# Kernel optimization log

Hardware: AMD Instinct MI355X
Metric: run time of the kernel (lower is better)

## Reference

```python
import jax, jax.numpy as jnp
import numpy as np

H = W = 64
ALPHA = 1.0
BETA = 100.0
LIMB_PAIRS = np.array([[0,1],[1,2],[2,3],[0,4],[4,5],[5,6],[0,7],[7,8],[8,9],[9,10],
                       [8,11],[11,12],[12,13],[8,14],[14,15],[15,16]])
P0 = LIMB_PAIRS[:, 0]
P1 = LIMB_PAIRS[:, 1]
_last = {}
for _l, _j in enumerate(P0):
    _last[int(_j)] = _l
J0 = np.array(list(_last.keys()))   # unique proximal joints
L0 = np.array(list(_last.values())) # last limb writing to each joint


def make_kernel(h, w, alpha):
    # replicates: coords = stack(meshgrid(arange(2h-1), arange(2w-1))).transpose(1,2) (h==w)
    ii, jj = jnp.meshgrid(jnp.arange(2 * h - 1), jnp.arange(2 * w - 1), indexing='ij')
    ker = jnp.stack([h - jj, w - ii], axis=0).astype(jnp.float32)  # (2, 2h-1, 2w-1)
    dist = jnp.linalg.norm(ker, axis=0, keepdims=True)
    dist = dist.at[0, h, w].set(1.0)
    return ker / dist ** (1.0 + alpha)


def corr_full(x, k):
    # x: (N, Cin, h, w); k: (Cout, Cin, 2h-1, 2w-1); 'same' correlation with pad h-1/w-1
    h, w = x.shape[-2:]
    return jax.lax.conv_general_dilated(x, k, (1, 1), ((h - 1, h - 1), (w - 1, w - 1)))


def heatmap_std(x, di=False):
    axes = (3, 4, 5) if di else (3, 4)
    return jnp.std(x, axis=axes, keepdims=True, ddof=1)


def heatmap_normalize(x, std, di=False):
    return x * std / (heatmap_std(x, di) + 1e-6)


def l2norm(v, axis):
    return v / jnp.maximum(jnp.linalg.norm(v, axis=axis, keepdims=True), 1e-12)


def soft_argmax(hm, beta):
    # hm: ... x h x w -> ... x 2 with (row_coord, col_coord) as in the torch code
    h, w = hm.shape[-2:]
    p = jax.nn.softmax(hm.reshape(hm.shape[:-2] + (-1,)) * beta, axis=-1).reshape(hm.shape)
    rows = jnp.arange(h, dtype=p.dtype)[:, None]
    cols = jnp.arange(w, dtype=p.dtype)[None, :]
    norm = p.sum((-2, -1))
    kp_x = (p * rows).sum((-2, -1)) / norm
    kp_y = (p * cols).sum((-2, -1)) / norm
    return jnp.stack((kp_x, kp_y), axis=-1)


def scale_pts(pts, image_shape, h, w):
    return jnp.stack((pts[..., 0] * image_shape[1] / w,
                      pts[..., 1] * image_shape[0] / h), axis=-1)


def cofix_forward(heatmaps, fields, Ps, Rs, Cs, image_shape, confs, vth1, vth2, pth1, pth2):
    bs, nv, nL, _, h, w = fields.shape
    nJ = heatmaps.shape[2]
    K = make_kernel(h, w, ALPHA)  # (2, 2h-1, 2w-1)

    heatmaps = heatmaps - jnp.mean(heatmaps, axis=(3, 4), keepdims=True)
    std_hm = heatmap_std(heatmaps, di=False)
    std_df = heatmap_std(fields, di=True)

    Hs = heatmaps[:, :, P1] - heatmaps[:, :, P0]  # (bs, nv, nL, h, w)
    # conv3d(kernel1, flipped Hs) == 'same' correlation of Hs with spatially-reversed K
    k1 = K[:, ::-1, ::-1][:, None]  # (2, 1, 2h-1, 2w-1)
    convs = corr_full(Hs.reshape(-1, 1, h, w), k1).reshape(bs, nv, nL, 2, h, w)

    coef = jax.nn.relu(jnp.sum(convs * fields[..., :2, :, :], axis=3, keepdims=True))
    fields_new = fields * coef

    fnorm = jnp.linalg.norm(fields, axis=3, keepdims=True)
    lvecs = l2norm(jnp.sum(fnorm * fields, axis=(4, 5)), axis=3)
    lpts = scale_pts(soft_argmax(fnorm[:, :, :, 0], BETA), image_shape, h, w)

    fnorm_new = jnp.linalg.norm(fields_new, axis=3, keepdims=True)
    lvecs_new = l2norm(jnp.sum(fnorm_new * fields_new, axis=(4, 5)), axis=3)
    lpts_new = scale_pts(soft_argmax(fnorm_new[:, :, :, 0], BETA), image_shape, h, w)

    # original code computes vec_selection(...) then overwrites: delta[:] = 0
    delta = jnp.zeros((bs, nv, nL, 1), dtype=heatmaps.dtype)
    comb_v = delta * lvecs_new + (1 - delta) * lvecs
    comb_p = delta * lpts_new + (1 - delta) * lpts

    d6 = delta[..., None, None]
    fields_c = heatmap_normalize(fields * (1 - d6) + fields_new * d6, std_df, di=True)

    # conv2d(kernel2, fields) then output spatial flip == 'same' correlation with K
    k2 = K[None]  # (1, 2, 2h-1, 2w-1)
    fds2jts = corr_full(fields_c[..., :2, :, :].reshape(-1, 2, h, w), k2)
    fds2jts = fds2jts.reshape(bs, nv, nL, h, w)
    prox_ = jax.nn.relu(-fds2jts)
    dist_ = jax.nn.relu(fds2jts)

    hms_new = heatmaps.at[:, :, J0].set(heatmaps[:, :, J0] * prox_[:, :, L0])
    hms_new = hms_new.at[:, :, P1].set(hms_new[:, :, P1] * dist_)
    hms_new = heatmap_normalize(hms_new, std_hm, di=False)

    kps = scale_pts(soft_argmax(heatmaps, BETA), image_shape, h, w)[..., None]
    kps_new = scale_pts(soft_argmax(hms_new, BETA), image_shape, h, w)[..., None]
    kps_new = jnp.where(jnp.isnan(kps_new), kps, kps_new)

    # sed_selection (reconstructed): keep refined kps where joint conf is high and
    # the refinement displacement is small.
    confs_j = confs[:, :, nL:]
    disp = jnp.linalg.norm((kps_new - kps)[..., 0], axis=-1)  # (bs, nv, nJ)
    sel = ((confs_j > pth1) & (disp < pth2)).astype(kps.dtype)[..., None, None]
    kps_combined = sel * kps_new + (1 - sel) * kps

    return kps_combined, comb_v, comb_p, fields_new, hms_new


def setup_inputs() -> dict:
    key = jax.random.key(0)
    ks = jax.random.split(key, 6)
    bs, nv, nJ, nL = 4, 4, 17, 16
    return {
        'heatmaps': jax.random.uniform(ks[0], (bs, nv, nJ, H, W), jnp.float32),
        'fields': jax.random.normal(ks[1], (bs, nv, nL, 3, H, W), jnp.float32),
        'Ps': jax.random.normal(ks[2], (bs, nv, 3, 4), jnp.float32),
        'Rs': jax.random.normal(ks[3], (bs, nv, 3, 3), jnp.float32),
        'Cs': jax.random.normal(ks[4], (bs, nv, 3, 1), jnp.float32),
        'image_shape': jnp.array([384, 384], jnp.int32),
        'confs': jax.random.uniform(ks[5], (bs, nv, nL + nJ), jnp.float32),
        'vth1': 0.5, 'vth2': 0.5, 'pth1': 0.1, 'pth2': 20.0,
    }


def reference(heatmaps, fields, Ps, Rs, Cs, image_shape, confs, vth1, vth2, pth1, pth2):
    return cofix_forward(heatmaps, fields, Ps, Rs, Cs, image_shape, confs,
                         vth1, vth2, pth1, pth2)
```

## Files before the change

### kernel.cpp

```cpp
#include <hip/hip_runtime.h>
#include <math.h>

#define TPB 1024
#define HTPB 256
#define NPIX 4096
#define NJ 17
#define NL 16
static constexpr float kBeta = 100.0f;
static constexpr float S2H = 0.70710678118654752f;

#define O_KPS 0
#define O_CV 544
#define O_CP 1312
#define O_FN 1824
#define O_HM 3147552
#define W_FDS 0
#define W_MEAN 1048576
#define W_STD 1048848
#define W_SF 1049120
#define W_W1 1049376
#define W_W2 1082144

__device__ __constant__ int c_P0[16] = {0,1,2,0,4,5,0,7,8,9,8,11,12,8,14,15};
__device__ __constant__ int c_P1[16] = {1,2,3,4,5,6,7,8,9,10,11,12,13,14,15,16};
__device__ __constant__ int c_proxL[17] = {6,1,2,-1,4,5,-1,7,13,9,-1,11,12,-1,14,15,-1};
__device__ __constant__ int c_distL[17] = {-1,0,1,2,3,4,5,6,7,8,9,10,11,12,13,14,15};

using cplx = float2;
__device__ inline cplx cadd(cplx a, cplx b){ return {a.x+b.x, a.y+b.y}; }
__device__ inline cplx csub(cplx a, cplx b){ return {a.x-b.x, a.y-b.y}; }
__device__ inline cplx cmul(cplx a, cplx w){ return {a.x*w.x - a.y*w.y, a.x*w.y + a.y*w.x}; }
__device__ inline cplx cmulc(cplx a, cplx w){ return {a.x*w.x + a.y*w.y, a.y*w.x - a.x*w.y}; }

__device__ __constant__ float2 W128BR[8] = {
  {1.f,0.f},
  {0.98078528040323044913f,-0.19509032201612826785f},
  {0.99518472667219688624f,-0.09801714032956060199f},
  {0.95694033573220886494f,-0.29028467725446236764f},
  {0.99879545620517239271f,-0.04906767432741801425f},
  {0.97003125319454399260f,-0.24298017990326388995f},
  {0.98917650996478097345f,-0.14673047445536175166f},
  {0.94154406518302077841f,-0.33688985339222005069f}
};
__device__ __constant__ float2 W16BR[8] = {
  {1.f,0.f},
  {0.f,-1.f},
  {0.70710678118654752440f,-0.70710678118654752440f},
  {-0.70710678118654752440f,-0.70710678118654752440f},
  {0.92387953251128675613f,-0.38268343236508977173f},
  {-0.38268343236508977173f,-0.92387953251128675613f},
  {0.38268343236508977173f,-0.92387953251128675613f},
  {-0.92387953251128675613f,-0.38268343236508977173f}
};

__device__ inline void bf8_tail(cplx t0, cplx t1, cplx t2, cplx t3,
                                cplx t4, cplx t5, cplx t6, cplx t7, cplx x[8]){
  cplx u0=cadd(t0,t2), u2=csub(t0,t2);
  cplx u1=cadd(t1,t3), d13=csub(t1,t3);
  cplx u3={d13.y,-d13.x};
  cplx u4=cadd(t4,t6), u6=csub(t4,t6);
  cplx u5=cadd(t5,t7), d57=csub(t5,t7);
  cplx u7={d57.y,-d57.x};
  x[0]=cadd(u0,u1); x[1]=csub(u0,u1);
  x[2]=cadd(u2,u3); x[3]=csub(u2,u3);
  x[4]=cadd(u4,u5); x[5]=csub(u4,u5);
  x[6]=cadd(u6,u7); x[7]=csub(u6,u7);
}
__device__ inline void bf8_fwd(cplx x[8]){
  cplx t0=cadd(x[0],x[4]), d4=csub(x[0],x[4]);
  cplx t1=cadd(x[1],x[5]), d5=csub(x[1],x[5]);
  cplx t2=cadd(x[2],x[6]), d6=csub(x[2],x[6]);
  cplx t3=cadd(x[3],x[7]), d7=csub(x[3],x[7]);
  cplx t5={S2H*(d5.x+d5.y), S2H*(d5.y-d5.x)};
  cplx t6={d6.y,-d6.x};
  cplx t7={S2H*(d7.y-d7.x), -S2H*(d7.x+d7.y)};
  bf8_tail(t0,t1,t2,t3,d4,t5,t6,t7,x);
}
__device__ inline void bf8_fwd_z(cplx x[8]){
  cplx t5={S2H*(x[1].x+x[1].y), S2H*(x[1].y-x[1].x)};
  cplx t6={x[2].y,-x[2].x};
  cplx t7={S2H*(x[3].y-x[3].x), -S2H*(x[3].x+x[3].y)};
  bf8_tail(x[0],x[1],x[2],x[3],x[0],t5,t6,t7,x);
}
__device__ inline void bf8_inv(cplx y[8]){
  cplx u0=cadd(y[0],y[1]), u1=csub(y[0],y[1]);
  cplx u2=cadd(y[2],y[3]), u3=csub(y[2],y[3]);
  cplx u4=cadd(y[4],y[5]), u5=csub(y[4],y[5]);
  cplx u6=cadd(y[6],y[7]), u7=csub(y[6],y[7]);
  cplx t0=cadd(u0,u2), t2=csub(u0,u2);
  cplx iu3={-u3.y,u3.x};
  cplx t1=cadd(u1,iu3), t3=csub(u1,iu3);
  cplx t4=cadd(u4,u6), t6=csub(u4,u6);
  cplx iu7={-u7.y,u7.x};
  cplx t5=cadd(u5,iu7), t7=csub(u5,iu7);
  y[0]=cadd(t0,t4); y[4]=csub(t0,t4);
  cplx w5={S2H*(t5.x-t5.y), S2H*(t5.x+t5.y)};
  y[1]=cadd(t1,w5); y[5]=csub(t1,w5);
  cplx w6={-t6.y,t6.x};
  y[2]=cadd(t2,w6); y[6]=csub(t2,w6);
  cplx w7={-S2H*(t7.x+t7.y), S2H*(t7.x-t7.y)};
  y[3]=cadd(t3,w7); y[7]=csub(t3,w7);
}

__device__ inline void fft16_fwd(cplx z[16]){
  cplx e[8], o[8];
  #pragma unroll
  for (int t=0;t<8;t++){ e[t]=z[2*t]; o[t]=z[2*t+1]; }
  bf8_fwd(e); bf8_fwd(o);
  #pragma unroll
  for (int p=0;p<8;p++){
    cplx vo = cmul(o[p], W16BR[p]);
    z[2*p]   = cadd(e[p], vo);
    z[2*p+1] = csub(e[p], vo);
  }
}
__device__ inline void fft16_inv(cplx z[16]){
  cplx e[8], o[8];
  #pragma unroll
  for (int p=0;p<8;p++){
    cplx a=z[2*p], b=z[2*p+1];
    e[p] = cadd(a,b);
    o[p] = cmulc(csub(a,b), W16BR[p]);
  }
  bf8_inv(e); bf8_inv(o);
  #pragma unroll
  for (int t=0;t<8;t++){ z[2*t]=e[t]; z[2*t+1]=o[t]; }
}

__device__ inline void twchainA(const cplx* TW, int j, cplx A[8]){
  cplx W1 = TW[j];
  cplx W2 = cmul(W1,W1);
  cplx W4 = cmul(W2,W2);
  cplx W6 = cmul(W4,W2);
  A[0] = {1.f,0.f}; A[1] = W4; A[2] = W2; A[3] = W6;
  A[4] = W1; A[5] = cmul(W4,W1); A[6] = cmul(W2,W1); A[7] = cmul(W6,W1);
}

__device__ inline int PH(int y, int m){ return (y<<6) | ((m ^ ((y&7)*9)) & 63); }

template<int NLINES, bool ZT>
__device__ void row_s1_fwd(float4* S4, const cplx* TW, int tid){
  if (tid < NLINES*8){
    const int L = tid>>3, m = tid&7;
    cplx xe[8], xo[8];
    #pragma unroll
    for (int t=0; t<(ZT?4:8); t++){
      float4 v = S4[PH(L, m+8*t)];
      xe[t]={v.x,v.y}; xo[t]={v.z,v.w};
    }
    if (ZT){ bf8_fwd_z(xe); bf8_fwd_z(xo); } else { bf8_fwd(xe); bf8_fwd(xo); }
    cplx A[8]; twchainA(TW, 2*m, A);
    #pragma unroll
    for (int p=0;p<8;p++){
      cplx B = cmul(A[p], W128BR[p]);
      cplx ve = cmul(xe[p], A[p]);
      cplx vo = cmul(xo[p], B);
      S4[PH(L, m+8*p)] = {ve.x, ve.y, vo.x, vo.y};
    }
  }
  __syncthreads();
}
__device__ void row_s1_inv(float4* S4, const cplx* TW, int tid){
  if (tid < 512){
    const int L = tid>>3, m = tid&7;
    cplx xe[8], xo[8];
    #pragma unroll
    for (int p=0;p<8;p++){
      float4 v = S4[PH(L, m+8*p)];
      xe[p]={v.x,v.y}; xo[p]={v.z,v.w};
    }
    cplx A[8]; twchainA(TW, 2*m, A);
    #pragma unroll
    for (int p=0;p<8;p++){
      cplx B = cmul(A[p], W128BR[p]);
      xe[p] = cmulc(xe[p], A[p]);
      xo[p] = cmulc(xo[p], B);
    }
    bf8_inv(xe); bf8_inv(xo);
    #pragma unroll
    for (int t=0;t<4;t++)
      S4[PH(L, m+8*t)] = {xe[t].x, xe[t].y, xo[t].x, xo[t].y};
  }
  __syncthreads();
}
template<int NLINES>
__device__ void row_s2_fwd(float4* S4, int tid){
  if (tid < NLINES*8){
    const int L = tid>>3, jb = tid&7;
    cplx z[16];
    #pragma unroll
    for (int k=0;k<8;k++){
      float4 v = S4[PH(L, jb*8+k)];
      z[2*k]={v.x,v.y}; z[2*k+1]={v.z,v.w};
    }
    fft16_fwd(z);
    #pragma unroll
    for (int k=0;k<8;k++)
      S4[PH(L, jb*8+k)] = {z[2*k].x, z[2*k].y, z[2*k+1].x, z[2*k+1].y};
  }
  __syncthreads();
}
__device__ void row_s2_inv(float4* S4, int tid){
  if (tid < 512){
    const int L = tid>>3, jb = tid&7;
    cplx z[16];
    #pragma unroll
    for (int k=0;k<8;k++){
      float4 v = S4[PH(L, jb*8+k)];
      z[2*k]={v.x,v.y}; z[2*k+1]={v.z,v.w};
    }
    fft16_inv(z);
    #pragma unroll
    for (int k=0;k<8;k++)
      S4[PH(L, jb*8+k)] = {z[2*k].x, z[2*k].y, z[2*k+1].x, z[2*k+1].y};
  }
  __syncthreads();
}
template<bool ZT>
__device__ void col_s1_fwd(float4* S4, const cplx* TW, int tid){
  const int cp = tid & 63, yj = tid >> 6;
  const int sl = (cp ^ ((yj&7)*9)) & 63;
  cplx xe[8], xo[8];
  #pragma unroll
  for (int t=0; t<(ZT?4:8); t++){
    float4 v = S4[((yj+16*t)<<6) | sl];
    xe[t]={v.x,v.y}; xo[t]={v.z,v.w};
  }
  if (ZT){ bf8_fwd_z(xe); bf8_fwd_z(xo); } else { bf8_fwd(xe); bf8_fwd(xo); }
  cplx A[8]; twchainA(TW, yj, A);
  #pragma unroll
  for (int p=0;p<8;p++){
    cplx ve = cmul(xe[p], A[p]);
    cplx vo = cmul(xo[p], A[p]);
    S4[((yj+16*p)<<6) | sl] = {ve.x, ve.y, vo.x, vo.y};
  }
  __syncthreads();
}
__device__ void col_s1_inv(float4* S4, const cplx* TW, int tid){
  const int cp = tid & 63, yj = tid >> 6;
  const int sl = (cp ^ ((yj&7)*9)) & 63;
  cplx xe[8], xo[8];
  #pragma unroll
  for (int p=0;p<8;p++){
    float4 v = S4[((yj+16*p)<<6) | sl];
    xe[p]={v.x,v.y}; xo[p]={v.z,v.w};
  }
  cplx A[8]; twchainA(TW, yj, A);
  #pragma unroll
  for (int p=0;p<8;p++){
    xe[p] = cmulc(xe[p], A[p]);
    xo[p] = cmulc(xo[p], A[p]);
  }
  bf8_inv(xe); bf8_inv(xo);
  #pragma unroll
  for (int t=0;t<4;t++)
    S4[((yj+16*t)<<6) | sl] = {xe[t].x, xe[t].y, xo[t].x, xo[t].y};
  __syncthreads();
}
__device__ void col_s2_fused(float4* S4, const cplx* __restrict__ Wg, int tid){
  cplx* Sc = (cplx*)S4;
  const int c = tid & 127, r = tid >> 7;
  const int ch = c & 1, cp = c >> 1;
  int ad[16];
  cplx z[16];
  #pragma unroll
  for (int i=0;i<16;i++){
    const int y = 16*r + i;
    ad[i] = ((((y<<6) | ((cp ^ ((y&7)*9)) & 63)) << 1) | ch);
    z[i] = Sc[ad[i]];
  }
  fft16_fwd(z);
  #pragma unroll
  for (int i=0;i<16;i++) z[i] = cmul(z[i], Wg[(16*r+i)*128 + c]);
  fft16_inv(z);
  #pragma unroll
  for (int i=0;i<16;i++) Sc[ad[i]] = z[i];
  __syncthreads();
}
__device__ void col_s2_fwd_store(float4* S4, cplx* __restrict__ Wo, int tid){
  cplx* Sc = (cplx*)S4;
  const int c = tid & 127, r = tid >> 7;
  const int ch = c & 1, cp = c >> 1;
  cplx z[16];
  #pragma unroll
  for (int i=0;i<16;i++){
    const int y = 16*r + i;
    z[i] = Sc[(((y<<6) | ((cp ^ ((y&7)*9)) & 63)) << 1) | ch];
  }
  fft16_fwd(z);
  const float scl = 1.0f / 16384.0f;
  #pragma unroll
  for (int i=0;i<16;i++) Wo[(16*r+i)*128 + c] = {z[i].x*scl, z[i].y*scl};
}

template<int N>
__device__ inline void reduce3n(float& a, float& b, float& c,
                                float* s0, float* s1, float* s2, int tid){
  s0[tid]=a; s1[tid]=b; s2[tid]=c; __syncthreads();
  for (int st = N/2; st; st >>= 1){
    if (tid < st){ s0[tid]+=s0[tid+st]; s1[tid]+=s1[tid+st]; s2[tid]+=s2[tid+st]; }
    __syncthreads();
  }
  a=s0[0]; b=s1[0]; c=s2[0]; __syncthreads();
}
template<int N>
__device__ inline float reduce_maxn(float v, float* s0, int tid){
  s0[tid]=v; __syncthreads();
  for (int st = N/2; st; st >>= 1){
    if (tid < st) s0[tid] = fmaxf(s0[tid], s0[tid+st]);
    __syncthreads();
  }
  const float r = s0[0]; __syncthreads();
  return r;
}

__device__ inline cplx wval(int r, int c, int which){
  const int dy = (r<64)? r : r-128;
  const int dx = (c<64)? c : c-128;
  float a, b;
  if (which==0){ a = 1.f-(float)dy; b = 1.f-(float)dx; }
  else         { a = 1.f+(float)dy; b = 1.f+(float)dx; }
  const float den = a*a + b*b;
  if (r==64 || c==64 || den<=0.f) return {0.f,0.f};
  const float inv = 1.f/den;
  return {a*inv, -b*inv};
}

__global__ __launch_bounds__(TPB,4) void pre_kernel(const float* __restrict__ heat,
                                                    const float* __restrict__ fields,
                                                    const int* __restrict__ ishape,
                                                    float* __restrict__ mean_hm,
                                                    float* __restrict__ std_hm,
                                                    float* __restrict__ sf,
                                                    float* __restrict__ W1,
                                                    float* __restrict__ W2,
                                                    float* __restrict__ out){
  __shared__ float4 S4[8192];
  __shared__ cplx TW[128];
  __shared__ float sA[TPB], sB[TPB], sC[TPB];
  const int tid = threadIdx.x;
  const int blk = blockIdx.x;
  if (blk < 272){
    const float* p = heat + (size_t)blk * NPIX;
    float s = 0.0f, s2 = 0.0f, d = 0.0f;
    for (int i = 0; i < 4; i++){
      const float x = p[tid + i*TPB];
      s += x; s2 += x*x;
    }
    reduce3n<TPB>(s, s2, d, sA, sB, sC, tid);
    if (tid == 0){
      const float mean = s / 4096.0f;
      const float var = (s2 - s*mean) / 4095.0f;
      mean_hm[blk] = mean;
      std_hm[blk] = sqrtf(fmaxf(var, 0.0f));
    }
  } else if (blk < 528){
    const int m = blk - 272;
    const float* f = fields + (size_t)m * 3 * NPIX;
    float s1 = 0.0f, s2 = 0.0f;
    float a0 = 0.0f, a1 = 0.0f, a2 = 0.0f;
    float fn[4];
    for (int i = 0; i < 4; i++){
      const int px = tid + i*TPB;
      const float f0 = f[px], f1 = f[NPIX+px], f2 = f[2*NPIX+px];
      s1 += f0+f1+f2; s2 += f0*f0+f1*f1+f2*f2;
      const float nn = sqrtf(f0*f0 + f1*f1 + f2*f2);
      fn[i] = nn;
      a0 += nn*f0; a1 += nn*f1; a2 += nn*f2;
    }
    {
      float t1 = s1, t2 = s2, t3 = 0.0f;
      reduce3n<TPB>(t1, t2, t3, sA, sB, sC, tid);
      if (tid == 0){
        const float var = (t2 - t1*t1/12288.0f) / 12287.0f;
        const float sd = sqrtf(fmaxf(var, 0.0f));
        sf[m] = sd / (sd + 1e-6f);
      }
    }
    reduce3n<TPB>(a0, a1, a2, sA, sB, sC, tid);
    float mx = fmaxf(fmaxf(fn[0],fn[1]), fmaxf(fn[2],fn[3]));
    mx = reduce_maxn<TPB>(mx, sA, tid);
    float Sm = 0.0f, Sx = 0.0f, Sy = 0.0f;
    for (int i = 0; i < 4; i++){
      const int px = tid + i*TPB;
      const float e = expf(kBeta * (fn[i] - mx));
      Sm += e; Sx += e * (float)(px>>6); Sy += e * (float)(px&63);
    }
    reduce3n<TPB>(Sm, Sx, Sy, sA, sB, sC, tid);
    if (tid == 0){
      float nrm = sqrtf(a0*a0 + a1*a1 + a2*a2);
      nrm = fmaxf(nrm, 1e-12f);
      out[O_CV + m*3 + 0] = a0/nrm;
      out[O_CV + m*3 + 1] = a1/nrm;
      out[O_CV + m*3 + 2] = a2/nrm;
      const float sxs = (float)ishape[1] / 64.0f;
      const float sys = (float)ishape[0] / 64.0f;
      out[O_CP + m*2 + 0] = Sx/Sm * sxs;
      out[O_CP + m*2 + 1] = Sy/Sm * sys;
    }
  } else {
    const int which = blk - 528;
    if (tid < 128){
      float s, c;
      sincosf(-6.283185307179586f * (float)tid / 128.0f, &s, &c);
      TW[tid] = {c, s};
    }
    for (int s = tid; s < 8192; s += TPB){
      const int y = s>>6, m = s&63;
      const cplx v0 = wval(y, 2*m, which);
      const cplx v1 = wval(y, 2*m+1, which);
      S4[PH(y, m)] = {v0.x, v0.y, v1.x, v1.y};
    }
    __syncthreads();
    row_s1_fwd<128,false>(S4, TW, tid);
    row_s2_fwd<128>(S4, tid);
    col_s1_fwd<false>(S4, TW, tid);
    col_s2_fwd_store(S4, (cplx*)((which==0)?W1:W2), tid);
  }
}

__global__ __launch_bounds__(TPB,4) void conv_kernel(const float* __restrict__ heat,
                                                     const float* __restrict__ mean_hm,
                                                     const float* __restrict__ fields,
                                                     const float* __restrict__ sf,
                                                     const float* __restrict__ W1g,
                                                     const float* __restrict__ W2g,
                                                     float* __restrict__ out_fn,
                                                     float* __restrict__ fds){
  __shared__ float4 S4[8192];
  __shared__ cplx TW[128];
  const int tid = threadIdx.x;
  const int n = blockIdx.x;
  const bool is1 = (n < 256);
  const int m_img = is1 ? n : (n - 256);
  if (tid < 128){
    float s, c;
    sincosf(-6.283185307179586f * (float)tid / 128.0f, &s, &c);
    TW[tid] = {c, s};
  }
  const float* f = fields + (size_t)m_img * 3 * NPIX;
  if (is1){
    const int bv = n >> 4, l = n & 15;
    const int j1 = bv*NJ + c_P1[l], j0 = bv*NJ + c_P0[l];
    const float* h1 = heat + (size_t)j1 * NPIX;
    const float* h0 = heat + (size_t)j0 * NPIX;
    const float dm = mean_hm[j1] - mean_hm[j0];
    for (int s = tid; s < 2048; s += TPB){
      const int y = s>>5, m = s&31;
      const int i = (y<<6) + 2*m;
      const float2 a = *(const float2*)(h1 + i);
      const float2 b = *(const float2*)(h0 + i);
      S4[PH(y, m)] = {a.x - b.x - dm, 0.f, a.y - b.y - dm, 0.f};
    }
  } else {
    for (int s = tid; s < 2048; s += TPB){
      const int y = s>>5, m = s&31;
      const int i = (y<<6) + 2*m;
      const float2 a = *(const float2*)(f + NPIX + i);
      const float2 b = *(const float2*)(f + i);
      S4[PH(y, m)] = {a.x, b.x, a.y, b.y};
    }
  }
  __syncthreads();
  row_s1_fwd<64,true>(S4, TW, tid);
  row_s2_fwd<64>(S4, tid);
  col_s1_fwd<true>(S4, TW, tid);
  col_s2_fused(S4, (const cplx*)(is1 ? W1g : W2g), tid);
  col_s1_inv(S4, TW, tid);
  row_s2_inv(S4, tid);
  row_s1_inv(S4, TW, tid);
  if (is1){
    float* o = out_fn + (size_t)n * 3 * NPIX;
    for (int s = tid; s < 2048; s += TPB){
      const int y = s>>5, m = s&31;
      const int i = (y<<6) + 2*m;
      const float4 v = S4[PH(y, m)];
      const float2 f0 = *(const float2*)(f + i);
      const float2 f1 = *(const float2*)(f + NPIX + i);
      const float2 f2 = *(const float2*)(f + 2*NPIX + i);
      const float cA = fmaxf(0.f, (-v.y)*f0.x + v.x*f1.x);
      const float cB = fmaxf(0.f, (-v.w)*f0.y + v.z*f1.y);
      *(float2*)(o + i)          = {f0.x*cA, f0.y*cB};
      *(float2*)(o + NPIX + i)   = {f1.x*cA, f1.y*cB};
      *(float2*)(o + 2*NPIX + i) = {f2.x*cA, f2.y*cB};
    }
  } else {
    const float sc = sf[m_img];
    float* o = fds + (size_t)m_img * NPIX;
    for (int s = tid; s < 2048; s += TPB){
      const int y = s>>5, m = s&31;
      const int i = (y<<6) + 2*m;
      const float4 v = S4[PH(y, m)];
      *(float2*)(o + i) = {v.x*sc, v.z*sc};
    }
  }
}

__global__ __launch_bounds__(HTPB) void hms_kernel(const float* __restrict__ heat,
                                                   const float* __restrict__ mean_hm,
                                                   const float* __restrict__ std_hm,
                                                   const float* __restrict__ fds,
                                                   const float* __restrict__ confs,
                                                   const int* __restrict__ ishape,
                                                   const float* __restrict__ pth1p,
                                                   const float* __restrict__ pth2p,
                                                   float* __restrict__ out){
  __shared__ float sA[HTPB], sB[HTPB], sC[HTPB];
  const int tid = threadIdx.x;
  const int idx = blockIdx.x;
  const int bv = idx / NJ, j = idx % NJ;
  const float* hp = heat + (size_t)idx * NPIX;
  const float mh = mean_hm[idx];
  const int pl = c_proxL[j], dl = c_distL[j];
  const float* fp = (pl >= 0) ? fds + (size_t)(bv*NL + pl) * NPIX : nullptr;
  const float* fd = (dl >= 0) ? fds + (size_t)(bv*NL + dl) * NPIX : nullptr;
  float ho[16], hn[16];
  float s = 0.0f, s2 = 0.0f, dummy = 0.0f;
  for (int i = 0; i < 16; i++){
    const int px = tid + i*HTPB;
    const float h = hp[px] - mh;
    ho[i] = h;
    float m = h;
    if (pl >= 0) m *= fmaxf(0.0f, -fp[px]);
    if (dl >= 0) m *= fmaxf(0.0f, fd[px]);
    hn[i] = m;
    s += m; s2 += m*m;
  }
  reduce3n<HTPB>(s, s2, dummy, sA, sB, sC, tid);
  const float var = (s2 - s*s/4096.0f) / 4095.0f;
  const float sdn = sqrtf(fmaxf(var, 0.0f));
  const float scale = std_hm[idx] / (sdn + 1e-6f);
  float* ohm = out + O_HM + (size_t)idx * NPIX;
  for (int i = 0; i < 16; i++){
    hn[i] *= scale;
    ohm[tid + i*HTPB] = hn[i];
  }
  float mo = -1e30f, mn = -1e30f;
  for (int i = 0; i < 16; i++){ mo = fmaxf(mo, ho[i]); mn = fmaxf(mn, hn[i]); }
  mo = reduce_maxn<HTPB>(mo, sA, tid);
  mn = reduce_maxn<HTPB>(mn, sA, tid);
  float So = 0.0f, Sxo = 0.0f, Syo = 0.0f;
  float Sn = 0.0f, Sxn = 0.0f, Syn = 0.0f;
  for (int i = 0; i < 16; i++){
    const int px = tid + i*HTPB;
    const float y = (float)(px >> 6), x = (float)(px & 63);
    const float eo = expf(kBeta * (ho[i] - mo));
    So += eo; Sxo += eo*y; Syo += eo*x;
    const float en = expf(kBeta * (hn[i] - mn));
    Sn += en; Sxn += en*y; Syn += en*x;
  }
  reduce3n<HTPB>(So, Sxo, Syo, sA, sB, sC, tid);
  reduce3n<HTPB>(Sn, Sxn, Syn, sA, sB, sC, tid);
  if (tid == 0){
    const float sxs = (float)ishape[1] / 64.0f;
    const float sys = (float)ishape[0] / 64.0f;
    const float kxo = Sxo/So * sxs, kyo = Syo/So * sys;
    float kxn = Sxn/Sn * sxs, kyn = Syn/Sn * sys;
    if (kxn != kxn) kxn = kxo;
    if (kyn != kyn) kyn = kyo;
    const float ddx = kxn - kxo, ddy = kyn - kyo;
    const float disp = sqrtf(ddx*ddx + ddy*ddy);
    const float conf = confs[bv*(NL+NJ) + NL + j];
    const bool sel = (conf > pth1p[0]) && (disp < pth2p[0]);
    out[O_KPS + idx*2 + 0] = sel ? kxn : kxo;
    out[O_KPS + idx*2 + 1] = sel ? kyn : kyo;
  }
}

extern "C" void kernel_launch(void* const* d_in, const int* in_sizes, int n_in,
                              void* d_out, int out_size, void* d_ws, size_t ws_size,
                              hipStream_t stream) {
  const float* heat   = (const float*)d_in[0];
  const float* fields = (const float*)d_in[1];
  const int*   ishape = (const int*)d_in[5];
  const float* confs  = (const float*)d_in[6];
  const float* pth1   = (const float*)d_in[9];
  const float* pth2   = (const float*)d_in[10];
  float* out = (float*)d_out;
  float* ws = (float*)d_ws;
  float* fds     = ws + W_FDS;
  float* mean_hm = ws + W_MEAN;
  float* std_hm  = ws + W_STD;
  float* sf      = ws + W_SF;
  float* W1      = ws + W_W1;
  float* W2      = ws + W_W2;

  hipLaunchKernelGGL(pre_kernel, dim3(530), dim3(TPB), 0, stream,
                     heat, fields, ishape, mean_hm, std_hm, sf, W1, W2, out);
  hipLaunchKernelGGL(conv_kernel, dim3(512), dim3(TPB), 0, stream,
                     heat, mean_hm, fields, sf, W1, W2, out + O_FN, fds);
  hipLaunchKernelGGL(hms_kernel, dim3(272), dim3(HTPB), 0, stream,
                     heat, mean_hm, std_hm, fds, confs, ishape, pth1, pth2, out);
}
```

Measured before the change: 159.8 us.

## Use wavefront-shuffle reductions, reorder pre-kernel blocks, split row FFT work per channel

```diff
diff --git a/kernel.cpp b/kernel.cpp
--- a/kernel.cpp
+++ b/kernel.cpp
@@ -160,27 +160,38 @@
   }
   __syncthreads();
 }
-__device__ void row_s1_inv(float4* S4, const cplx* TW, int tid){
-  if (tid < 512){
-    const int L = tid>>3, m = tid&7;
-    cplx xe[8], xo[8];
-    #pragma unroll
-    for (int p=0;p<8;p++){
-      float4 v = S4[PH(L, m+8*p)];
-      xe[p]={v.x,v.y}; xo[p]={v.z,v.w};
-    }
-    cplx A[8]; twchainA(TW, 2*m, A);
-    #pragma unroll
-    for (int p=0;p<8;p++){
-      cplx B = cmul(A[p], W128BR[p]);
-      xe[p] = cmulc(xe[p], A[p]);
-      xo[p] = cmulc(xo[p], B);
-    }
-    bf8_inv(xe); bf8_inv(xo);
-    #pragma unroll
-    for (int t=0;t<4;t++)
-      S4[PH(L, m+8*t)] = {xe[t].x, xe[t].y, xo[t].x, xo[t].y};
-  }
+__device__ void row_s1_fwd64a(float4* S4, const cplx* TW, int tid){
+  float2* Sc = (float2*)S4;
+  const int u = tid >> 1, ch = tid & 1;
+  const int L = u >> 3, m = u & 7;
+  cplx x[8];
+  #pragma unroll
+  for (int t=0;t<4;t++) x[t] = Sc[2*PH(L, m+8*t) + ch];
+  bf8_fwd_z(x);
+  cplx A[8]; twchainA(TW, 2*m, A);
+  #pragma unroll
+  for (int p=0;p<8;p++){
+    const cplx w = ch ? cmul(A[p], W128BR[p]) : A[p];
+    Sc[2*PH(L, m+8*p) + ch] = cmul(x[p], w);
+  }
+  __syncthreads();
+}
+__device__ void row_s1_inv64a(float4* S4, const cplx* TW, int tid){
+  float2* Sc = (float2*)S4;
+  const int u = tid >> 1, ch = tid & 1;
+  const int L = u >> 3, m = u & 7;
+  cplx x[8];
+  #pragma unroll
+  for (int p=0;p<8;p++) x[p] = Sc[2*PH(L, m+8*p) + ch];
+  cplx A[8]; twchainA(TW, 2*m, A);
+  #pragma unroll
+  for (int p=0;p<8;p++){
+    const cplx w = ch ? cmul(A[p], W128BR[p]) : A[p];
+    x[p] = cmulc(x[p], w);
+  }
+  bf8_inv(x);
+  #pragma unroll
+  for (int t=0;t<4;t++) Sc[2*PH(L, m+8*t) + ch] = x[t];
   __syncthreads();
 }
 template<int NLINES>
@@ -262,7 +273,9 @@
   const int c = tid & 127, r = tid >> 7;
   const int ch = c & 1, cp = c >> 1;
   int ad[16];
-  cplx z[16];
+  cplx z[16], wv[16];
+  #pragma unroll
+  for (int i=0;i<16;i++) wv[i] = Wg[(16*r+i)*128 + c];
   #pragma unroll
   for (int i=0;i<16;i++){
     const int y = 16*r + i;
@@ -271,7 +284,7 @@
   }
   fft16_fwd(z);
   #pragma unroll
-  for (int i=0;i<16;i++) z[i] = cmul(z[i], Wg[(16*r+i)*128 + c]);
+  for (int i=0;i<16;i++) z[i] = cmul(z[i], wv[i]);
   fft16_inv(z);
   #pragma unroll
   for (int i=0;i<16;i++) Sc[ad[i]] = z[i];
@@ -293,24 +306,48 @@
   for (int i=0;i<16;i++) Wo[(16*r+i)*128 + c] = {z[i].x*scl, z[i].y*scl};
 }
 
-template<int N>
-__device__ inline void reduce3n(float& a, float& b, float& c,
-                                float* s0, float* s1, float* s2, int tid){
-  s0[tid]=a; s1[tid]=b; s2[tid]=c; __syncthreads();
-  for (int st = N/2; st; st >>= 1){
-    if (tid < st){ s0[tid]+=s0[tid+st]; s1[tid]+=s1[tid+st]; s2[tid]+=s2[tid+st]; }
-    __syncthreads();
-  }
-  a=s0[0]; b=s1[0]; c=s2[0]; __syncthreads();
-}
-template<int N>
-__device__ inline float reduce_maxn(float v, float* s0, int tid){
-  s0[tid]=v; __syncthreads();
-  for (int st = N/2; st; st >>= 1){
-    if (tid < st) s0[tid] = fmaxf(s0[tid], s0[tid+st]);
-    __syncthreads();
-  }
-  const float r = s0[0]; __syncthreads();
+__device__ inline float wred(float v){
+  #pragma unroll
+  for (int o=32;o;o>>=1) v += __shfl_xor(v, o, 64);
+  return v;
+}
+__device__ inline float wredmax(float v){
+  #pragma unroll
+  for (int o=32;o;o>>=1) v = fmaxf(v, __shfl_xor(v, o, 64));
+  return v;
+}
+template<int NW>
+__device__ inline void bred3(float& a, float& b, float& c,
+                             float* s0, float* s1, float* s2, int tid){
+  a = wred(a); b = wred(b); c = wred(c);
+  const int w = tid >> 6;
+  if ((tid & 63) == 0){ s0[w]=a; s1[w]=b; s2[w]=c; }
+  __syncthreads();
+  if (tid == 0){
+    float A=0.f, B=0.f, C=0.f;
+    #pragma unroll
+    for (int i=0;i<NW;i++){ A+=s0[i]; B+=s1[i]; C+=s2[i]; }
+    s0[0]=A; s1[0]=B; s2[0]=C;
+  }
+  __syncthreads();
+  a = s0[0]; b = s1[0]; c = s2[0];
+  __syncthreads();
+}
+template<int NW>
+__device__ inline float bredmax(float v, float* s0, int tid){
+  v = wredmax(v);
+  const int w = tid >> 6;
+  if ((tid & 63) == 0) s0[w] = v;
+  __syncthreads();
+  if (tid == 0){
+    float M = s0[0];
+    #pragma unroll
+    for (int i=1;i<NW;i++) M = fmaxf(M, s0[i]);
+    s0[0] = M;
+  }
+  __syncthreads();
+  const float r = s0[0];
+  __syncthreads();
   return r;
 }
 
@@ -337,29 +374,50 @@
                                                     float* __restrict__ out){
   __shared__ float4 S4[8192];
   __shared__ cplx TW[128];
-  __shared__ float sA[TPB], sB[TPB], sC[TPB];
+  __shared__ float sA[16], sB[16], sC[16];
   const int tid = threadIdx.x;
   const int blk = blockIdx.x;
-  if (blk < 272){
-    const float* p = heat + (size_t)blk * NPIX;
+  if (blk < 2){
+    const int which = blk;
+    if (tid < 128){
+      float s, c;
+      sincosf(-6.283185307179586f * (float)tid / 128.0f, &s, &c);
+      TW[tid] = {c, s};
+    }
+    for (int s = tid; s < 8192; s += TPB){
+      const int y = s>>6, m = s&63;
+      const cplx v0 = wval(y, 2*m, which);
+      const cplx v1 = wval(y, 2*m+1, which);
+      S4[PH(y, m)] = {v0.x, v0.y, v1.x, v1.y};
+    }
+    __syncthreads();
+    row_s1_fwd<128,false>(S4, TW, tid);
+    row_s2_fwd<128>(S4, tid);
+    col_s1_fwd<false>(S4, TW, tid);
+    col_s2_fwd_store(S4, (cplx*)((which==0)?W1:W2), tid);
+  } else if (blk < 274){
+    const int n = blk - 2;
+    const float* p = heat + (size_t)n * NPIX;
     float s = 0.0f, s2 = 0.0f, d = 0.0f;
+    #pragma unroll
     for (int i = 0; i < 4; i++){
       const float x = p[tid + i*TPB];
       s += x; s2 += x*x;
     }
-    reduce3n<TPB>(s, s2, d, sA, sB, sC, tid);
+    bred3<16>(s, s2, d, sA, sB, sC, tid);
     if (tid == 0){
       const float mean = s / 4096.0f;
       const float var = (s2 - s*mean) / 4095.0f;
-      mean_hm[blk] = mean;
-      std_hm[blk] = sqrtf(fmaxf(var, 0.0f));
-    }
-  } else if (blk < 528){
-    const int m = blk - 272;
+      mean_hm[n] = mean;
+      std_hm[n] = sqrtf(fmaxf(var, 0.0f));
+    }
+  } else {
+    const int m = blk - 274;
     const float* f = fields + (size_t)m * 3 * NPIX;
     float s1 = 0.0f, s2 = 0.0f;
     float a0 = 0.0f, a1 = 0.0f, a2 = 0.0f;
     float fn[4];
+    #pragma unroll
     for (int i = 0; i < 4; i++){
       const int px = tid + i*TPB;
       const float f0 = f[px], f1 = f[NPIX+px], f2 = f[2*NPIX+px];
@@ -370,23 +428,24 @@
     }
     {
       float t1 = s1, t2 = s2, t3 = 0.0f;
-      reduce3n<TPB>(t1, t2, t3, sA, sB, sC, tid);
+      bred3<16>(t1, t2, t3, sA, sB, sC, tid);
       if (tid == 0){
         const float var = (t2 - t1*t1/12288.0f) / 12287.0f;
         const float sd = sqrtf(fmaxf(var, 0.0f));
         sf[m] = sd / (sd + 1e-6f);
       }
     }
-    reduce3n<TPB>(a0, a1, a2, sA, sB, sC, tid);
+    bred3<16>(a0, a1, a2, sA, sB, sC, tid);
     float mx = fmaxf(fmaxf(fn[0],fn[1]), fmaxf(fn[2],fn[3]));
-    mx = reduce_maxn<TPB>(mx, sA, tid);
+    mx = bredmax<16>(mx, sA, tid);
     float Sm = 0.0f, Sx = 0.0f, Sy = 0.0f;
+    #pragma unroll
     for (int i = 0; i < 4; i++){
       const int px = tid + i*TPB;
       const float e = expf(kBeta * (fn[i] - mx));
       Sm += e; Sx += e * (float)(px>>6); Sy += e * (float)(px&63);
     }
-    reduce3n<TPB>(Sm, Sx, Sy, sA, sB, sC, tid);
+    bred3<16>(Sm, Sx, Sy, sA, sB, sC, tid);
     if (tid == 0){
       float nrm = sqrtf(a0*a0 + a1*a1 + a2*a2);
       nrm = fmaxf(nrm, 1e-12f);
@@ -398,24 +457,6 @@
       out[O_CP + m*2 + 0] = Sx/Sm * sxs;
       out[O_CP + m*2 + 1] = Sy/Sm * sys;
     }
-  } else {
-    const int which = blk - 528;
-    if (tid < 128){
-      float s, c;
-      sincosf(-6.283185307179586f * (float)tid / 128.0f, &s, &c);
-      TW[tid] = {c, s};
-    }
-    for (int s = tid; s < 8192; s += TPB){
-      const int y = s>>6, m = s&63;
-      const cplx v0 = wval(y, 2*m, which);
-      const cplx v1 = wval(y, 2*m+1, which);
-      S4[PH(y, m)] = {v0.x, v0.y, v1.x, v1.y};
-    }
-    __syncthreads();
-    row_s1_fwd<128,false>(S4, TW, tid);
-    row_s2_fwd<128>(S4, tid);
-    col_s1_fwd<false>(S4, TW, tid);
-    col_s2_fwd_store(S4, (cplx*)((which==0)?W1:W2), tid);
   }
 }
 
@@ -431,16 +472,16 @@
   __shared__ cplx TW[128];
   const int tid = threadIdx.x;
   const int n = blockIdx.x;
-  const bool is1 = (n < 256);
-  const int m_img = is1 ? n : (n - 256);
+  const bool is2 = (n < 256);
+  const int m_img = is2 ? n : (n - 256);
   if (tid < 128){
     float s, c;
     sincosf(-6.283185307179586f * (float)tid / 128.0f, &s, &c);
     TW[tid] = {c, s};
   }
   const float* f = fields + (size_t)m_img * 3 * NPIX;
-  if (is1){
-    const int bv = n >> 4, l = n & 15;
+  if (!is2){
+    const int bv = m_img >> 4, l = m_img & 15;
     const int j1 = bv*NJ + c_P1[l], j0 = bv*NJ + c_P0[l];
     const float* h1 = heat + (size_t)j1 * NPIX;
     const float* h0 = heat + (size_t)j0 * NPIX;
@@ -462,15 +503,15 @@
     }
   }
   __syncthreads();
-  row_s1_fwd<64,true>(S4, TW, tid);
+  row_s1_fwd64a(S4, TW, tid);
   row_s2_fwd<64>(S4, tid);
   col_s1_fwd<true>(S4, TW, tid);
-  col_s2_fused(S4, (const cplx*)(is1 ? W1g : W2g), tid);
+  col_s2_fused(S4, (const cplx*)(is2 ? W2g : W1g), tid);
   col_s1_inv(S4, TW, tid);
   row_s2_inv(S4, tid);
-  row_s1_inv(S4, TW, tid);
-  if (is1){
-    float* o = out_fn + (size_t)n * 3 * NPIX;
+  row_s1_inv64a(S4, TW, tid);
+  if (!is2){
+    float* o = out_fn + (size_t)m_img * 3 * NPIX;
     for (int s = tid; s < 2048; s += TPB){
       const int y = s>>5, m = s&31;
       const int i = (y<<6) + 2*m;
@@ -505,7 +546,7 @@
                                                    const float* __restrict__ pth1p,
                                                    const float* __restrict__ pth2p,
                                                    float* __restrict__ out){
-  __shared__ float sA[HTPB], sB[HTPB], sC[HTPB];
+  __shared__ float sA[4], sB[4], sC[4];
   const int tid = threadIdx.x;
   const int idx = blockIdx.x;
   const int bv = idx / NJ, j = idx % NJ;
@@ -516,6 +557,7 @@
   const float* fd = (dl >= 0) ? fds + (size_t)(bv*NL + dl) * NPIX : nullptr;
   float ho[16], hn[16];
   float s = 0.0f, s2 = 0.0f, dummy = 0.0f;
+  #pragma unroll
   for (int i = 0; i < 16; i++){
     const int px = tid + i*HTPB;
     const float h = hp[px] - mh;
@@ -526,21 +568,24 @@
     hn[i] = m;
     s += m; s2 += m*m;
   }
-  reduce3n<HTPB>(s, s2, dummy, sA, sB, sC, tid);
+  bred3<4>(s, s2, dummy, sA, sB, sC, tid);
   const float var = (s2 - s*s/4096.0f) / 4095.0f;
   const float sdn = sqrtf(fmaxf(var, 0.0f));
   const float scale = std_hm[idx] / (sdn + 1e-6f);
   float* ohm = out + O_HM + (size_t)idx * NPIX;
+  #pragma unroll
   for (int i = 0; i < 16; i++){
     hn[i] *= scale;
     ohm[tid + i*HTPB] = hn[i];
   }
   float mo = -1e30f, mn = -1e30f;
+  #pragma unroll
   for (int i = 0; i < 16; i++){ mo = fmaxf(mo, ho[i]); mn = fmaxf(mn, hn[i]); }
-  mo = reduce_maxn<HTPB>(mo, sA, tid);
-  mn = reduce_maxn<HTPB>(mn, sA, tid);
+  mo = bredmax<4>(mo, sA, tid);
+  mn = bredmax<4>(mn, sA, tid);
   float So = 0.0f, Sxo = 0.0f, Syo = 0.0f;
   float Sn = 0.0f, Sxn = 0.0f, Syn = 0.0f;
+  #pragma unroll
   for (int i = 0; i < 16; i++){
     const int px = tid + i*HTPB;
     const float y = (float)(px >> 6), x = (float)(px & 63);
@@ -549,8 +594,8 @@
     const float en = expf(kBeta * (hn[i] - mn));
     Sn += en; Sxn += en*y; Syn += en*x;
   }
-  reduce3n<HTPB>(So, Sxo, Syo, sA, sB, sC, tid);
-  reduce3n<HTPB>(Sn, Sxn, Syn, sA, sB, sC, tid);
+  bred3<4>(So, Sxo, Syo, sA, sB, sC, tid);
+  bred3<4>(Sn, Sxn, Syn, sA, sB, sC, tid);
   if (tid == 0){
     const float sxs = (float)ishape[1] / 64.0f;
     const float sys = (float)ishape[0] / 64.0f;
```

Result: faster. 153.0 us (-4.3%).
